# Kernel optimization log

Hardware: AMD Instinct MI355X
Metric: run time of the kernel (lower is better)

The kernel has to match this reference:

```python
import jax, jax.numpy as jnp
import numpy as np

B, N, C, K = 8, 4096, 64, 30
EPS_BN = 1e-5
TINY = 1e-20  # guards sqrt/atan2 at the exact self-neighbor (rel == 0)


def _knn(p, k):
    xx = jnp.sum(p * p, axis=1)  # [B, N]
    pd = 2.0 * jnp.einsum('bdn,bdm->bnm', p, p) - xx[:, :, None] - xx[:, None, :]
    return jax.lax.top_k(pd, k)[1]  # [B, N, k]


def _bn(h, g, b):
    # BatchNorm1d in training mode: biased batch stats over all dims but channel (last)
    mu = jnp.mean(h, axis=(0, 1, 2), keepdims=True)
    var = jnp.var(h, axis=(0, 1, 2), keepdims=True)
    return (h - mu) * jax.lax.rsqrt(var + EPS_BN) * g + b


def _forward(x_loc, x, W1, g1, b1, W2, g2, b2, W3, g3, b3, k):
    Bsz = x.shape[0]
    idx = _knn(x_loc, k)                       # [B, N, k]
    bidx = jnp.arange(Bsz)[:, None, None]
    pts = x_loc.transpose(0, 2, 1)             # [B, N, 3]
    rel = pts[bidx, idx] - pts[:, :, None, :]  # [B, N, k, 3] neighbor - center
    xr, yr, zr = rel[..., 0], rel[..., 1], rel[..., 2]
    sxy2 = xr * xr + yr * yr
    r2 = sxy2 + zr * zr
    rho = jnp.sqrt(jnp.maximum(r2, TINY))
    sxy = jnp.sqrt(jnp.maximum(sxy2, TINY))
    deg_r = r2 < TINY
    deg_p = sxy2 < TINY
    theta = jnp.arctan2(jnp.where(deg_r, 0.0, zr), jnp.where(deg_r, 1.0, sxy))
    phi = jnp.arctan2(jnp.where(deg_p, 0.0, yr), jnp.where(deg_p, 1.0, xr))
    sph = jnp.stack([rho, theta, phi], axis=-1)            # [B, N, k, 3]
    # torch car2sph averages across the 3 spherical channels (dim=-1)
    feat = jnp.concatenate([sph, sph - jnp.mean(sph, axis=-1, keepdims=True)], axis=-1)  # [B,N,k,6]
    lrelu = lambda h: jax.nn.leaky_relu(h, 0.2)
    h = lrelu(_bn(feat @ W1.T, g1, b1))        # [B, N, k, 6]
    h = lrelu(_bn(h @ W2.T, g2, b2))           # [B, N, k, 3]
    h = lrelu(_bn(h @ W3.T, g3, b3))           # [B, N, k, 1]
    att = jax.nn.softmax(h[..., 0], axis=-1)   # [B, N, k]
    xk = x.transpose(0, 2, 1)[bidx, idx]       # [B, N, k, C]
    agg = jnp.einsum('bnkc,bnk->bnc', xk, att)
    return x + agg.transpose(0, 2, 1)          # [B, C, N]


def setup_inputs() -> dict:
    key = jax.random.key(0)
    ks = jax.random.split(key, 12)
    return {
        'x_loc': jax.random.normal(ks[0], (B, 3, N), jnp.float32),
        'x': jax.random.normal(ks[1], (B, C, N), jnp.float32),
        'W1': jax.random.normal(ks[2], (6, 6), jnp.float32) * 0.4,
        'g1': 1.0 + 0.1 * jax.random.normal(ks[3], (6,), jnp.float32),
        'b1': 0.1 * jax.random.normal(ks[4], (6,), jnp.float32),
        'W2': jax.random.normal(ks[5], (3, 6), jnp.float32) * 0.4,
        'g2': 1.0 + 0.1 * jax.random.normal(ks[6], (3,), jnp.float32),
        'b2': 0.1 * jax.random.normal(ks[7], (3,), jnp.float32),
        'W3': jax.random.normal(ks[8], (1, 3), jnp.float32) * 0.4,
        'g3': 1.0 + 0.1 * jax.random.normal(ks[9], (1,), jnp.float32),
        'b3': 0.1 * jax.random.normal(ks[10], (1,), jnp.float32),
        'k': K,
    }


def reference(x_loc, x, W1, g1, b1, W2, g2, b2, W3, g3, b3, k):
    return _forward(x_loc, x, W1, g1, b1, W2, g2, b2, W3, g3, b3, k)
```

## Files before the change

kernel.cpp:

```cpp
#include <hip/hip_runtime.h>
#include <math.h>

#define NPTS 4096
#define NB   8
#define NC   64
#define KSEL 30
#define NROWS (NB * NPTS * KSEL)
#define CNT_F 983040.0f
#define SURVZ 3840
#define P23_BLOCKS 960
#define P23_STRIDE (P23_BLOCKS * 256)

static __device__ __forceinline__ unsigned long long shfl_xor_u64(unsigned long long v, int lx) {
    int lo = __shfl_xor((int)(unsigned)(v & 0xFFFFFFFFULL), lx, 64);
    int hi = __shfl_xor((int)(unsigned)(v >> 32), lx, 64);
    return ((unsigned long long)(unsigned)hi << 32) | (unsigned)lo;
}

template <int NM>
static __device__ __forceinline__ void slot_reduce(const float* __restrict__ acc,
                                                   float* __restrict__ sSum, int tid) {
    if (tid < 64) {
        float pm[NM];
#pragma unroll
        for (int m = 0; m < NM; ++m) pm[m] = acc[m * 64 + tid];
#pragma unroll
        for (int o = 32; o > 0; o >>= 1) {
#pragma unroll
            for (int m = 0; m < NM; ++m) pm[m] += __shfl_xor(pm[m], o, 64);
        }
        if (tid == 0) {
#pragma unroll
            for (int m = 0; m < NM; ++m) sSum[m] = pm[m];
        }
    }
}

static __device__ __forceinline__ void bn1_params(const float* __restrict__ sSum,
                                                  const float* __restrict__ W1,
                                                  const float* __restrict__ g1,
                                                  const float* __restrict__ b1,
                                                  float* __restrict__ sPar, int tid) {
    if (tid < 6) {
        const float invN = 1.0f / CNT_F;
        const float m0 = sSum[0] * invN, m1 = sSum[1] * invN, m2 = sSum[2] * invN;
        const float E00 = sSum[3] * invN, E01 = sSum[4] * invN, E02 = sSum[5] * invN;
        const float E11 = sSum[6] * invN, E12 = sSum[7] * invN, E22 = sSum[8] * invN;
        const float* w = W1 + tid * 6;
        const float third = (w[3] + w[4] + w[5]) * (1.0f / 3.0f);
        const float a0 = w[0] + w[3] - third;
        const float a1 = w[1] + w[4] - third;
        const float a2 = w[2] + w[5] - third;
        const float mu = a0 * m0 + a1 * m1 + a2 * m2;
        const float E2 = a0 * a0 * E00 + a1 * a1 * E11 + a2 * a2 * E22 +
                         2.0f * (a0 * a1 * E01 + a0 * a2 * E02 + a1 * a2 * E12);
        const float var = E2 - mu * mu;
        const float sc = g1[tid] / sqrtf(var + 1e-5f);
        sPar[tid] = sc;
        sPar[6 + tid] = b1[tid] - mu * sc;
    }
}

static __device__ __forceinline__ void bn2_params(const float* __restrict__ sSum,
                                                  const float* __restrict__ W2,
                                                  const float* __restrict__ g2,
                                                  const float* __restrict__ b2,
                                                  float* __restrict__ sPar, int tid) {
    if (tid < 3) {
        const float invN = 1.0f / CNT_F;
        float Eh[6];
#pragma unroll
        for (int d = 0; d < 6; ++d) Eh[d] = sSum[d] * invN;
        float M[6][6];
        int q = 6;
#pragma unroll
        for (int a2 = 0; a2 < 6; ++a2)
#pragma unroll
            for (int b2_ = a2; b2_ < 6; ++b2_) {
                const float v = sSum[q++] * invN;
                M[a2][b2_] = v; M[b2_][a2] = v;
            }
        const float* w = W2 + tid * 6;
        float mu = 0.0f;
#pragma unroll
        for (int d = 0; d < 6; ++d) mu += w[d] * Eh[d];
        float E2 = 0.0f;
#pragma unroll
        for (int a2 = 0; a2 < 6; ++a2)
#pragma unroll
            for (int b2_ = 0; b2_ < 6; ++b2_) E2 += w[a2] * w[b2_] * M[a2][b2_];
        const float var = E2 - mu * mu;
        const float sc = g2[tid] / sqrtf(var + 1e-5f);
        sPar[12 + tid] = sc;
        sPar[15 + tid] = b2[tid] - mu * sc;
    }
}

static __device__ __forceinline__ void bn3_params(const float* __restrict__ sSum,
                                                  const float* __restrict__ W3,
                                                  const float* __restrict__ g3,
                                                  const float* __restrict__ b3,
                                                  float* __restrict__ sPar, int tid) {
    if (tid == 0) {
        const float invN = 1.0f / CNT_F;
        const float Eh0 = sSum[0] * invN, Eh1 = sSum[1] * invN, Eh2 = sSum[2] * invN;
        const float M00 = sSum[3] * invN, M01 = sSum[4] * invN, M02 = sSum[5] * invN;
        const float M11 = sSum[6] * invN, M12 = sSum[7] * invN, M22 = sSum[8] * invN;
        const float w0 = W3[0], w1 = W3[1], w2 = W3[2];
        const float mu = w0 * Eh0 + w1 * Eh1 + w2 * Eh2;
        const float E2 = w0 * w0 * M00 + w1 * w1 * M11 + w2 * w2 * M22 +
                         2.0f * (w0 * w1 * M01 + w0 * w2 * M02 + w1 * w2 * M12);
        const float var = E2 - mu * mu;
        const float sc = g3[0] / sqrtf(var + 1e-5f);
        sPar[0] = sc;
        sPar[1] = b3[0] - mu * sc;
    }
}

static __device__ __forceinline__ void mlp_h1(float s0, float s1, float s2,
                                              const float* __restrict__ W1,
                                              const float* __restrict__ sPar,
                                              float* __restrict__ h1) {
    const float mean = (s0 + s1 + s2) * (1.0f / 3.0f);
    const float f[6] = {s0, s1, s2, s0 - mean, s1 - mean, s2 - mean};
#pragma unroll
    for (int c = 0; c < 6; ++c) {
        float a = 0.0f;
#pragma unroll
        for (int d = 0; d < 6; ++d) a = fmaf(W1[c * 6 + d], f[d], a);
        const float z = fmaf(a, sPar[c], sPar[6 + c]);
        h1[c] = z >= 0.0f ? z : 0.2f * z;
    }
}

static __device__ __forceinline__ void mlp_h2(const float* __restrict__ h1,
                                              const float* __restrict__ W2,
                                              const float* __restrict__ sPar,
                                              float* __restrict__ h2) {
#pragma unroll
    for (int c = 0; c < 3; ++c) {
        float a = 0.0f;
#pragma unroll
        for (int d = 0; d < 6; ++d) a = fmaf(W2[c * 6 + d], h1[d], a);
        const float z = fmaf(a, sPar[12 + c], sPar[15 + c]);
        h2[c] = z >= 0.0f ? z : 0.2f * z;
    }
}

__global__ __launch_bounds__(512, 4) void knn_k(const float* __restrict__ xloc,
                                                int* __restrict__ idx_out,
                                                float* __restrict__ sph,
                                                float* __restrict__ accM) {
    __shared__ float4 pts[NPTS];
    __shared__ float msc[72];

    const int tid  = threadIdx.x;
    const int lane = tid & 63;
    const int wv   = tid >> 6;
    const int b    = blockIdx.y;
    const int n    = (blockIdx.x << 3) + wv;

    const float* xb = xloc + (size_t)b * (3 * NPTS);
    for (int i = tid; i < NPTS; i += 512) {
        const float x = xb[i], y = xb[NPTS + i], z = xb[2 * NPTS + i];
        const float xx = __fadd_rn(__fadd_rn(__fmul_rn(x, x), __fmul_rn(y, y)), __fmul_rn(z, z));
        pts[i] = make_float4(x, y, z, xx);
    }
    __syncthreads();

    const float4 q = pts[n];

    unsigned K[64];
    unsigned lm = 0;
#pragma unroll
    for (int t = 0; t < 64; ++t) {
        const float4 c = pts[lane + (t << 6)];
        const float dt = __fadd_rn(__fadd_rn(__fmul_rn(q.x, c.x), __fmul_rn(q.y, c.y)), __fmul_rn(q.z, c.z));
        const float pd = __fsub_rn(__fsub_rn(__fmul_rn(2.0f, dt), q.w), c.w);
        const unsigned u = __float_as_uint(pd);
        const unsigned key = u ^ ((unsigned)((int)u >> 31) | 0x80000000u);
        K[t] = key;
        lm = key > lm ? key : lm;
    }

    unsigned v = lm;
#pragma unroll
    for (int k = 2; k <= 64; k <<= 1) {
#pragma unroll
        for (int j2 = k >> 1; j2 > 0; j2 >>= 1) {
            const unsigned o = (unsigned)__shfl_xor((int)v, j2, 64);
            const bool keepmax = ((lane & j2) == 0) == ((lane & k) == 0);
            const unsigned mx = v > o ? v : o;
            const unsigned mn = v > o ? o : v;
            v = keepmax ? mx : mn;
        }
    }
    const unsigned tau = (unsigned)__shfl((int)v, 30, 64);

    __syncthreads();

    unsigned long long* surv = ((unsigned long long*)(pts + SURVZ)) + (wv << 6);
    surv[lane] = 0ULL;

    unsigned total = 0;
#pragma unroll
    for (int t = 0; t < 64; ++t) {
        const bool p = (K[t] >= tau);
        const unsigned long long m = __ballot(p);
        if (p) {
            const unsigned pos = total + (unsigned)__popcll(m & ((1ULL << lane) - 1ULL));
            if (pos < 64u) {
                const unsigned j = (unsigned)(lane + (t << 6));
                surv[pos] = ((unsigned long long)K[t] << 32) | (unsigned)(~j);
            }
        }
        total += (unsigned)__popcll(m);
    }
    __threadfence_block();

    const int bn = (b << 12) + n;
    const size_t obase = (size_t)bn * KSEL;
    int jn = 0;

    if (total <= 64u) {
        unsigned long long s = surv[lane];
#pragma unroll
        for (int k = 2; k <= 64; k <<= 1) {
#pragma unroll
            for (int j2 = k >> 1; j2 > 0; j2 >>= 1) {
                const unsigned long long o = shfl_xor_u64(s, j2);
                const bool keepmax = ((lane & j2) == 0) == ((lane & k) == 0);
                const unsigned long long mx = s > o ? s : o;
                const unsigned long long mn = s > o ? o : s;
                s = keepmax ? mx : mn;
            }
        }
        jn = (int)(~(unsigned)s) & (NPTS - 1);
        if (lane >= KSEL) jn = 0;
    } else {
        unsigned P = 0;
        for (int bit = 31; bit >= 0; --bit) {
            const unsigned cand = P | (1u << bit);
            int c = 0;
#pragma unroll
            for (int t = 0; t < 64; ++t) c += (K[t] >= cand) ? 1 : 0;
#pragma unroll
            for (int o = 32; o > 0; o >>= 1) c += __shfl_xor(c, o, 64);
            if (c >= KSEL) P = cand;
        }
        int* sj = (int*)surv;
        int emitted = 0;
#pragma unroll
        for (int t = 0; t < 64; ++t) {
            const bool g = (K[t] > P);
            const unsigned long long m = __ballot(g);
            if (g) {
                const int pos = emitted + (int)__popcll(m & ((1ULL << lane) - 1ULL));
                if (pos < KSEL) sj[pos] = lane + (t << 6);
            }
            emitted += (int)__popcll(m);
        }
#pragma unroll
        for (int t = 0; t < 64; ++t) {
            const bool e_ = (K[t] == P);
            const unsigned long long m = __ballot(e_);
            const int before = (int)__popcll(m & ((1ULL << lane) - 1ULL));
            if (e_ && (emitted + before) < KSEL) sj[emitted + before] = lane + (t << 6);
            emitted += (int)__popcll(m);
        }
        __threadfence_block();
        if (lane < KSEL) jn = sj[lane];
    }

    float s0 = 0.0f, s1 = 0.0f, s2 = 0.0f;
    if (lane < KSEL) {
        idx_out[obase + lane] = jn;
        float cx, cy, cz;
        if (jn >= SURVZ) {
            cx = xb[jn]; cy = xb[NPTS + jn]; cz = xb[2 * NPTS + jn];
        } else {
            const float4 c = pts[jn];
            cx = c.x; cy = c.y; cz = c.z;
        }
        const float xr = cx - q.x, yr = cy - q.y, zr = cz - q.z;
        const float sxy2 = xr * xr + yr * yr;
        const float r2   = sxy2 + zr * zr;
        const float rho  = sqrtf(fmaxf(r2, 1e-20f));
        const float sxy  = sqrtf(fmaxf(sxy2, 1e-20f));
        const bool dr = r2 < 1e-20f;
        const bool dp = sxy2 < 1e-20f;
        const float theta = atan2f(dr ? 0.0f : zr, dr ? 1.0f : sxy);
        const float phi   = atan2f(dp ? 0.0f : yr, dp ? 1.0f : xr);
        sph[obase + lane]             = rho;
        sph[NROWS + obase + lane]     = theta;
        sph[2 * NROWS + obase + lane] = phi;
        s0 = rho; s1 = theta; s2 = phi;
    }

    float mom[9] = {s0, s1, s2, s0 * s0, s0 * s1, s0 * s2, s1 * s1, s1 * s2, s2 * s2};
#pragma unroll
    for (int o = 32; o > 0; o >>= 1) {
#pragma unroll
        for (int m = 0; m < 9; ++m) mom[m] += __shfl_xor(mom[m], o, 64);
    }
    if (lane == 0) {
#pragma unroll
        for (int m = 0; m < 9; ++m) msc[wv * 9 + m] = mom[m];
    }
    __syncthreads();
    if (tid < 9) {
        float t_ = 0.0f;
#pragma unroll
        for (int w = 0; w < 8; ++w) t_ += msc[w * 9 + tid];
        atomicAdd(&accM[tid * 64 + ((blockIdx.y * 512 + blockIdx.x) & 63)], t_);
    }
}

__global__ __launch_bounds__(256) void p2_k(const float* __restrict__ sph,
                                            const float* __restrict__ x,
                                            float* __restrict__ xT,
                                            const float* __restrict__ W1,
                                            const float* __restrict__ g1,
                                            const float* __restrict__ b1,
                                            const float* __restrict__ accM,
                                            float* __restrict__ acc2) {
    __shared__ float sSum[9];
    __shared__ float sPar[12];
    __shared__ float red[4][27];
    __shared__ float tile[64][65];
    const int tid = threadIdx.x;
    slot_reduce<9>(accM, sSum, tid);
    __syncthreads();
    bn1_params(sSum, W1, g1, b1, sPar, tid);
    __syncthreads();

    float m27[27];
#pragma unroll
    for (int m = 0; m < 27; ++m) m27[m] = 0.0f;
#pragma unroll
    for (int s = 0; s < 4; ++s) {
        const size_t r = (size_t)blockIdx.x * 256 + tid + (size_t)s * P23_STRIDE;
        const float s0 = sph[r], s1 = sph[NROWS + r], s2 = sph[2 * NROWS + r];
        float h1[6];
        mlp_h1(s0, s1, s2, W1, sPar, h1);
        int qq = 6;
#pragma unroll
        for (int a2 = 0; a2 < 6; ++a2) {
            m27[a2] += h1[a2];
#pragma unroll
            for (int b2_ = a2; b2_ < 6; ++b2_) m27[qq++] += h1[a2] * h1[b2_];
        }
    }
#pragma unroll
    for (int o = 32; o > 0; o >>= 1) {
#pragma unroll
        for (int m = 0; m < 27; ++m) m27[m] += __shfl_xor(m27[m], o, 64);
    }
    const int lane = tid & 63, wv = tid >> 6;
    if (lane == 0) {
#pragma unroll
        for (int m = 0; m < 27; ++m) red[wv][m] = m27[m];
    }
    __syncthreads();
    if (tid < 27) {
        const float v = red[0][tid] + red[1][tid] + red[2][tid] + red[3][tid];
        atomicAdd(&acc2[tid * 64 + (blockIdx.x & 63)], v);
    }

    if (blockIdx.x < 512) {
        const int b  = blockIdx.x >> 6;
        const int n0 = (blockIdx.x & 63) << 6;
        const int tx = tid & 63;
        const int ty = tid >> 6;
        const float* xb = x + ((size_t)b << 18);
#pragma unroll
        for (int i = 0; i < 16; ++i) {
            const int c = (i << 2) + ty;
            tile[c][tx] = xb[((size_t)c << 12) + n0 + tx];
        }
        __syncthreads();
        float* ob = xT + ((size_t)b << 18);
#pragma unroll
        for (int i = 0; i < 16; ++i) {
            const int nl = (i << 2) + ty;
            ob[((size_t)(n0 + nl) << 6) + tx] = tile[tx][nl];
        }
    }
}

__global__ __launch_bounds__(256) void p3_k(const float* __restrict__ sph,
                                            const float* __restrict__ W1,
                                            const float* __restrict__ g1,
                                            const float* __restrict__ b1,
                                            const float* __restrict__ W2,
                                            const float* __restrict__ g2,
                                            const float* __restrict__ b2,
                                            const float* __restrict__ W3,
                                            const float* __restrict__ accM,
                                            const float* __restrict__ acc2,
                                            float* __restrict__ acc3,
                                            float* __restrict__ y3) {
    __shared__ float sSum[27];
    __shared__ float sPar[18];
    __shared__ float red[4][9];
    const int tid = threadIdx.x;
    slot_reduce<9>(accM, sSum, tid);
    __syncthreads();
    bn1_params(sSum, W1, g1, b1, sPar, tid);
    __syncthreads();
    slot_reduce<27>(acc2, sSum, tid);
    __syncthreads();
    bn2_params(sSum, W2, g2, b2, sPar, tid);
    __syncthreads();

    const float w30 = W3[0], w31 = W3[1], w32 = W3[2];

    float m9[9];
#pragma unroll
    for (int m = 0; m < 9; ++m) m9[m] = 0.0f;
#pragma unroll
    for (int s = 0; s < 4; ++s) {
        const size_t r = (size_t)blockIdx.x * 256 + tid + (size_t)s * P23_STRIDE;
        const float s0 = sph[r], s1 = sph[NROWS + r], s2 = sph[2 * NROWS + r];
        float h1[6], h2[3];
        mlp_h1(s0, s1, s2, W1, sPar, h1);
        mlp_h2(h1, W2, sPar, h2);
        y3[r] = fmaf(w30, h2[0], fmaf(w31, h2[1], w32 * h2[2]));
        m9[0] += h2[0]; m9[1] += h2[1]; m9[2] += h2[2];
        m9[3] += h2[0] * h2[0]; m9[4] += h2[0] * h2[1]; m9[5] += h2[0] * h2[2];
        m9[6] += h2[1] * h2[1]; m9[7] += h2[1] * h2[2]; m9[8] += h2[2] * h2[2];
    }
#pragma unroll
    for (int o = 32; o > 0; o >>= 1) {
#pragma unroll
        for (int m = 0; m < 9; ++m) m9[m] += __shfl_xor(m9[m], o, 64);
    }
    const int lane = tid & 63, wv = tid >> 6;
    if (lane == 0) {
#pragma unroll
        for (int m = 0; m < 9; ++m) red[wv][m] = m9[m];
    }
    __syncthreads();
    if (tid < 9) {
        const float v = red[0][tid] + red[1][tid] + red[2][tid] + red[3][tid];
        atomicAdd(&acc3[tid * 64 + (blockIdx.x & 63)], v);
    }
}

__global__ __launch_bounds__(256) void p4_k(const float* __restrict__ y3,
                                            const int* __restrict__ idx,
                                            const float* __restrict__ x,
                                            const float* __restrict__ xT,
                                            const float* __restrict__ W3,
                                            const float* __restrict__ g3,
                                            const float* __restrict__ b3,
                                            const float* __restrict__ acc3,
                                            float* __restrict__ out) {
    __shared__ float sSum[9];
    __shared__ float sPar[2];
    __shared__ float agg[32][65];
    const int tid = threadIdx.x;
    slot_reduce<9>(acc3, sSum, tid);
    __syncthreads();
    bn3_params(sSum, W3, g3, b3, sPar, tid);
    __syncthreads();
    const float sc3 = sPar[0], tb3 = sPar[1];

    const int lane = tid & 63, wv = tid >> 6;
    const int b    = blockIdx.x & 7;
    const int n0   = (blockIdx.x >> 3) << 5;
    const int p0   = (b << 12) + n0;
    const float* xTb = xT + ((size_t)b << 18);

    for (int i = 0; i < 8; ++i) {
        const int pl = (wv << 3) + i;
        const int p  = p0 + pl;
        float a = -3.4e38f;
        int jn = 0;
        if (lane < KSEL) {
            const size_t r = (size_t)p * KSEL + lane;
            const float z = fmaf(y3[r], sc3, tb3);
            a = z >= 0.0f ? z : 0.2f * z;
            jn = idx[r];
        }
        float mx = a;
#pragma unroll
        for (int o = 32; o > 0; o >>= 1) mx = fmaxf(mx, __shfl_xor(mx, o, 64));
        const float e = (lane < KSEL) ? expf(a - mx) : 0.0f;
        float se = e;
#pragma unroll
        for (int o = 32; o > 0; o >>= 1) se += __shfl_xor(se, o, 64);
        const float w = e / se;

        float acc0 = 0.0f, acc1 = 0.0f;
#pragma unroll
        for (int t = 0; t < KSEL; t += 2) {
            const int   j0 = __shfl(jn, t, 64);
            const float w0 = __shfl(w, t, 64);
            const int   j1 = __shfl(jn, t + 1, 64);
            const float w1 = __shfl(w, t + 1, 64);
            acc0 = fmaf(w0, xTb[((size_t)j0 << 6) + lane], acc0);
            acc1 = fmaf(w1, xTb[((size_t)j1 << 6) + lane], acc1);
        }
        agg[pl][lane] = acc0 + acc1;
    }
    __syncthreads();

    const float* xb = x + ((size_t)b << 18);
    float* ob = out + ((size_t)b << 18);
    const int nl = tid & 31, cb = tid >> 5;
#pragma unroll
    for (int i = 0; i < 8; ++i) {
        const int c = (i << 3) + cb;
        const size_t off = ((size_t)c << 12) + n0 + nl;
        ob[off] = xb[off] + agg[nl][c];
    }
}

extern "C" void kernel_launch(void* const* d_in, const int* in_sizes, int n_in,
                              void* d_out, int out_size, void* d_ws, size_t ws_size,
                              hipStream_t stream) {
    const float* x_loc = (const float*)d_in[0];
    const float* x     = (const float*)d_in[1];
    const float* W1    = (const float*)d_in[2];
    const float* g1    = (const float*)d_in[3];
    const float* b1    = (const float*)d_in[4];
    const float* W2    = (const float*)d_in[5];
    const float* g2    = (const float*)d_in[6];
    const float* b2    = (const float*)d_in[7];
    const float* W3    = (const float*)d_in[8];
    const float* g3    = (const float*)d_in[9];
    const float* b3    = (const float*)d_in[10];
    float* out = (float*)d_out;

    float* accM = (float*)d_ws;
    float* acc2 = accM + 576;
    float* acc3 = acc2 + 1728;
    float* sph  = acc3 + 576;
    int*   idx  = (int*)(sph + 3 * (size_t)NROWS);
    float* y3   = (float*)(idx + NROWS);
    float* xT   = y3 + NROWS;

    hipMemsetAsync(d_ws, 0, 11520, stream);

    knn_k<<<dim3(NPTS / 8, NB), 512, 0, stream>>>(x_loc, idx, sph, accM);
    p2_k<<<P23_BLOCKS, 256, 0, stream>>>(sph, x, xT, W1, g1, b1, accM, acc2);
    p3_k<<<P23_BLOCKS, 256, 0, stream>>>(sph, W1, g1, b1, W2, g2, b2, W3, accM, acc2, acc3, y3);
    p4_k<<<(NB * NPTS) / 32, 256, 0, stream>>>(y3, idx, x, xT, W3, g3, b3, acc3, out);
}
```

Baseline: 254.7 us.

## Recompute kNN distances instead of holding 64 keys in registers

The 64-entry per-lane key array is dropped. Distances are recomputed from shared memory on a second pass, and in the rare fallback radix-select path, to cut register pressure and possibly raise occupancy. Survivor lists move into a dedicated shared array rather than aliasing the tail of the point table. This removes the block-wide barrier and the global-memory fallback load for high-index neighbors. The cost is roughly doubled distance arithmetic and LDS reads in the common path, and the fallback path now runs far more LDS traffic.

```diff
diff --git a/kernel.cpp b/kernel.cpp
--- a/kernel.cpp
+++ b/kernel.cpp
@@ -7,7 +7,6 @@
 #define KSEL 30
 #define NROWS (NB * NPTS * KSEL)
 #define CNT_F 983040.0f
-#define SURVZ 3840
 #define P23_BLOCKS 960
 #define P23_STRIDE (P23_BLOCKS * 256)
 
@@ -15,6 +14,11 @@
     int lo = __shfl_xor((int)(unsigned)(v & 0xFFFFFFFFULL), lx, 64);
     int hi = __shfl_xor((int)(unsigned)(v >> 32), lx, 64);
     return ((unsigned long long)(unsigned)hi << 32) | (unsigned)lo;
+}
+
+static __device__ __forceinline__ unsigned f2key(float f) {
+    const unsigned u = __float_as_uint(f);
+    return u ^ ((unsigned)((int)u >> 31) | 0x80000000u);
 }
 
 template <int NM>
@@ -152,6 +156,7 @@
                                                 float* __restrict__ sph,
                                                 float* __restrict__ accM) {
     __shared__ float4 pts[NPTS];
+    __shared__ unsigned long long survA[8][64];
     __shared__ float msc[72];
 
     const int tid  = threadIdx.x;
@@ -170,48 +175,45 @@
 
     const float4 q = pts[n];
 
-    unsigned K[64];
-    unsigned lm = 0;
+    float pmax = -3.4e38f;
 #pragma unroll
     for (int t = 0; t < 64; ++t) {
         const float4 c = pts[lane + (t << 6)];
         const float dt = __fadd_rn(__fadd_rn(__fmul_rn(q.x, c.x), __fmul_rn(q.y, c.y)), __fmul_rn(q.z, c.z));
         const float pd = __fsub_rn(__fsub_rn(__fmul_rn(2.0f, dt), q.w), c.w);
-        const unsigned u = __float_as_uint(pd);
-        const unsigned key = u ^ ((unsigned)((int)u >> 31) | 0x80000000u);
-        K[t] = key;
-        lm = key > lm ? key : lm;
-    }
-
-    unsigned v = lm;
+        pmax = fmaxf(pmax, pd);
+    }
+
+    float v = pmax;
 #pragma unroll
     for (int k = 2; k <= 64; k <<= 1) {
 #pragma unroll
         for (int j2 = k >> 1; j2 > 0; j2 >>= 1) {
-            const unsigned o = (unsigned)__shfl_xor((int)v, j2, 64);
+            const float o = __shfl_xor(v, j2, 64);
             const bool keepmax = ((lane & j2) == 0) == ((lane & k) == 0);
-            const unsigned mx = v > o ? v : o;
-            const unsigned mn = v > o ? o : v;
-            v = keepmax ? mx : mn;
-        }
-    }
-    const unsigned tau = (unsigned)__shfl((int)v, 30, 64);
-
-    __syncthreads();
-
-    unsigned long long* surv = ((unsigned long long*)(pts + SURVZ)) + (wv << 6);
+            v = keepmax ? fmaxf(v, o) : fminf(v, o);
+        }
+    }
+    const float tau = __shfl(v, 30, 64);
+
+    __asm__ __volatile__("" ::: "memory");
+
+    unsigned long long* surv = survA[wv];
     surv[lane] = 0ULL;
 
     unsigned total = 0;
 #pragma unroll
     for (int t = 0; t < 64; ++t) {
-        const bool p = (K[t] >= tau);
+        const float4 c = pts[lane + (t << 6)];
+        const float dt = __fadd_rn(__fadd_rn(__fmul_rn(q.x, c.x), __fmul_rn(q.y, c.y)), __fmul_rn(q.z, c.z));
+        const float pd = __fsub_rn(__fsub_rn(__fmul_rn(2.0f, dt), q.w), c.w);
+        const bool p = (pd >= tau);
         const unsigned long long m = __ballot(p);
         if (p) {
             const unsigned pos = total + (unsigned)__popcll(m & ((1ULL << lane) - 1ULL));
             if (pos < 64u) {
                 const unsigned j = (unsigned)(lane + (t << 6));
-                surv[pos] = ((unsigned long long)K[t] << 32) | (unsigned)(~j);
+                surv[pos] = ((unsigned long long)f2key(pd) << 32) | (unsigned)(~j);
             }
         }
         total += (unsigned)__popcll(m);
@@ -238,21 +240,24 @@
         jn = (int)(~(unsigned)s) & (NPTS - 1);
         if (lane >= KSEL) jn = 0;
     } else {
-        unsigned P = 0;
+        auto keyf = [&](int j) -> unsigned {
+            const float4 c = pts[j];
+            const float dt = __fadd_rn(__fadd_rn(__fmul_rn(q.x, c.x), __fmul_rn(q.y, c.y)), __fmul_rn(q.z, c.z));
+            const float pd = __fsub_rn(__fsub_rn(__fmul_rn(2.0f, dt), q.w), c.w);
+            return f2key(pd);
+        };
+        unsigned Pv = 0;
         for (int bit = 31; bit >= 0; --bit) {
-            const unsigned cand = P | (1u << bit);
+            const unsigned cand = Pv | (1u << bit);
             int c = 0;
-#pragma unroll
-            for (int t = 0; t < 64; ++t) c += (K[t] >= cand) ? 1 : 0;
-#pragma unroll
+            for (int t = 0; t < 64; ++t) c += (keyf(lane + (t << 6)) >= cand) ? 1 : 0;
             for (int o = 32; o > 0; o >>= 1) c += __shfl_xor(c, o, 64);
-            if (c >= KSEL) P = cand;
+            if (c >= KSEL) Pv = cand;
         }
         int* sj = (int*)surv;
         int emitted = 0;
-#pragma unroll
         for (int t = 0; t < 64; ++t) {
-            const bool g = (K[t] > P);
+            const bool g = (keyf(lane + (t << 6)) > Pv);
             const unsigned long long m = __ballot(g);
             if (g) {
                 const int pos = emitted + (int)__popcll(m & ((1ULL << lane) - 1ULL));
@@ -260,9 +265,8 @@
             }
             emitted += (int)__popcll(m);
         }
-#pragma unroll
         for (int t = 0; t < 64; ++t) {
-            const bool e_ = (K[t] == P);
+            const bool e_ = (keyf(lane + (t << 6)) == Pv);
             const unsigned long long m = __ballot(e_);
             const int before = (int)__popcll(m & ((1ULL << lane) - 1ULL));
             if (e_ && (emitted + before) < KSEL) sj[emitted + before] = lane + (t << 6);
@@ -275,14 +279,8 @@
     float s0 = 0.0f, s1 = 0.0f, s2 = 0.0f;
     if (lane < KSEL) {
         idx_out[obase + lane] = jn;
-        float cx, cy, cz;
-        if (jn >= SURVZ) {
-            cx = xb[jn]; cy = xb[NPTS + jn]; cz = xb[2 * NPTS + jn];
-        } else {
-            const float4 c = pts[jn];
-            cx = c.x; cy = c.y; cz = c.z;
-        }
-        const float xr = cx - q.x, yr = cy - q.y, zr = cz - q.z;
+        const float4 c = pts[jn];
+        const float xr = c.x - q.x, yr = c.y - q.y, zr = c.z - q.z;
         const float sxy2 = xr * xr + yr * yr;
         const float r2   = sxy2 + zr * zr;
         const float rho  = sqrtf(fmaxf(r2, 1e-20f));
```

New measurement: 274.2 us. 7.7% more time.
